# Kernel optimization log

Hardware: AMD Instinct MI355X
Metric: run time of the kernel (lower is better)

## Reference

```python
import jax, jax.numpy as jnp
import numpy as np

B, T, D, K = 4, 2048, 1024, 64


def _spectral_filters(seq_len, k):
    # Hankel matrix Z_ij = 2 / ((i+j)^3 - (i+j)), top-k eig-pairs scaled by sigma^0.25
    e = np.arange(1, seq_len + 1, dtype=np.float64)
    ipj = e[:, None] + e[None, :]
    Z = 2.0 / (ipj ** 3 - ipj)
    sig, phi = np.linalg.eigh(Z)
    sig_k = np.clip(sig[-k:], 1e-9, None)
    return (phi[:, -k:] * sig_k ** 0.25).astype(np.float32)


def setup_inputs() -> dict:
    key = jax.random.key(0)
    ks = jax.random.split(key, 6)
    filt = jnp.asarray(_spectral_filters(T, K))  # [T, K]
    inp = {
        "x": jax.random.normal(ks[0], (B, T, D), dtype=jnp.float32),
        "W_pre": jax.random.normal(ks[1], (D, T), dtype=jnp.float32) / np.sqrt(D),
        "b_pre": jnp.zeros((T,), dtype=jnp.float32),
        "Q_filt": filt,
        "K_filt": jnp.array(filt),
        "W_v": jax.random.normal(ks[2], (D, K), dtype=jnp.float32) / np.sqrt(D),
        "b_v": jnp.zeros((K,), dtype=jnp.float32),
        "W_o": jax.random.normal(ks[3], (K, D), dtype=jnp.float32) / np.sqrt(K),
        "b_o": jnp.zeros((D,), dtype=jnp.float32),
        "decay": jnp.ones((T,), dtype=jnp.float32),
    }
    return inp


def reference(x, W_pre, b_pre, Q_filt, K_filt, W_v, b_v, W_o, b_o, decay):
    # pre-projection d_model -> seq_len (since d_model != seq_len)
    x_proj = x @ W_pre + b_pre                      # [B, T, T]
    Q = jnp.einsum('bti,ik->btk', x_proj, Q_filt)   # [B, T, K]
    Kf = jnp.einsum('bti,ik->btk', x_proj, K_filt)  # [B, T, K]
    V = x @ W_v + b_v                               # [B, T, K]
    # outer-product state with per-timestep decay, prefix-summed over time
    Z = jnp.einsum('btp,btn->btpn', V, Kf) * decay[None, :, None, None]  # [B,T,K,K]
    H = jnp.cumsum(Z, axis=1)                       # [B, T, K, K]
    Y = jnp.einsum('btk,btkn->btn', Q, H)           # [B, T, K]
    return Y @ W_o + b_o                            # [B, T, D]
```

## Files before the change

kernel.cpp:

```cpp
#include <hip/hip_runtime.h>

#define TS 2048
#define DM 1024
#define KD 64
#define NB 4

#define WTH_OFF 0
#define WTL_OFF 98304
#define BC_OFF  196608
#define QG_OFF  196864
#define P_OFF   1769728
#define PF_OFF  (P_OFF)
#define ST_OFF  (P_OFF)
#define O_OFF   8061184
#define YB_OFF  9109760

typedef __attribute__((ext_vector_type(8))) short bf16x8;
typedef __attribute__((ext_vector_type(4))) float f32x4;

__device__ __forceinline__ ushort f2bf(float f) {
  unsigned u = __float_as_uint(f);
  unsigned r = u + 0x7FFFu + ((u >> 16) & 1u);
  return (ushort)(r >> 16);
}
__device__ __forceinline__ float bf2f(ushort h) {
  return __uint_as_float(((unsigned)h) << 16);
}

__global__ __launch_bounds__(256) void k_prep(
    const float* __restrict__ W_pre, const float* __restrict__ Qf,
    const float* __restrict__ Kf, float* __restrict__ Pf) {
  const int d0 = blockIdx.x * 64;
  const int f = blockIdx.y;
  const int ks = blockIdx.z;
  const float* __restrict__ F = f ? Kf : Qf;
  const int tid = threadIdx.x;
  const int wave = tid >> 6, lane = tid & 63;
  const int quad = lane >> 4, l15 = lane & 15;
  __shared__ ushort As[64 * 72];
  __shared__ ushort Bs[64 * 72];
  f32x4 acc[4];
#pragma unroll
  for (int nt = 0; nt < 4; ++nt) acc[nt] = (f32x4){0.f, 0.f, 0.f, 0.f};

  const int ra = tid >> 3;
  const int c4 = (tid & 7) * 4;
  float4 aw[2];
  float bw[8];
  int t0 = ks * 128;
#pragma unroll
  for (int i = 0; i < 2; ++i)
    aw[i] = *(const float4*)&W_pre[(size_t)(d0 + i * 32 + ra) * TS + t0 + c4];
#pragma unroll
  for (int h = 0; h < 2; ++h)
#pragma unroll
    for (int u = 0; u < 4; ++u)
      bw[h * 4 + u] = F[(size_t)(t0 + (wave + 4 * h) * 4 + u) * KD + lane];

  for (int step = 0; step < 4; ++step) {
    __syncthreads();
#pragma unroll
    for (int i = 0; i < 2; ++i) {
      const int r = i * 32 + ra;
      const float4 v = aw[i];
      const ushort h0 = f2bf(v.x), h1 = f2bf(v.y), h2 = f2bf(v.z), h3 = f2bf(v.w);
      *(ushort4*)&As[r * 72 + c4] = make_ushort4(h0, h1, h2, h3);
      *(ushort4*)&As[r * 72 + 32 + c4] = make_ushort4(
          f2bf(v.x - bf2f(h0)), f2bf(v.y - bf2f(h1)),
          f2bf(v.z - bf2f(h2)), f2bf(v.w - bf2f(h3)));
    }
#pragma unroll
    for (int h = 0; h < 2; ++h) {
      const int gg = wave + 4 * h;
      ushort hh[4], ll[4];
#pragma unroll
      for (int u = 0; u < 4; ++u) {
        hh[u] = f2bf(bw[h * 4 + u]);
        ll[u] = f2bf(bw[h * 4 + u] - bf2f(hh[u]));
      }
      *(ushort4*)&Bs[lane * 72 + gg * 4] = make_ushort4(hh[0], hh[1], hh[2], hh[3]);
      *(ushort4*)&Bs[lane * 72 + 32 + gg * 4] = make_ushort4(ll[0], ll[1], ll[2], ll[3]);
    }
    __syncthreads();
    if (step < 3) {
      const int t1 = t0 + 32;
#pragma unroll
      for (int i = 0; i < 2; ++i)
        aw[i] = *(const float4*)&W_pre[(size_t)(d0 + i * 32 + ra) * TS + t1 + c4];
#pragma unroll
      for (int h = 0; h < 2; ++h)
#pragma unroll
        for (int u = 0; u < 4; ++u)
          bw[h * 4 + u] = F[(size_t)(t1 + (wave + 4 * h) * 4 + u) * KD + lane];
    }
    const ushort* ap = &As[(wave * 16 + l15) * 72 + quad * 8];
    const bf16x8 a_h = *(const bf16x8*)ap;
    const bf16x8 a_l = *(const bf16x8*)(ap + 32);
#pragma unroll
    for (int nt = 0; nt < 4; ++nt) {
      const ushort* bp = &Bs[(nt * 16 + l15) * 72 + quad * 8];
      const bf16x8 b_h = *(const bf16x8*)bp;
      const bf16x8 b_l = *(const bf16x8*)(bp + 32);
      acc[nt] = __builtin_amdgcn_mfma_f32_16x16x32_bf16(a_h, b_h, acc[nt], 0, 0, 0);
      acc[nt] = __builtin_amdgcn_mfma_f32_16x16x32_bf16(a_h, b_l, acc[nt], 0, 0, 0);
      acc[nt] = __builtin_amdgcn_mfma_f32_16x16x32_bf16(a_l, b_h, acc[nt], 0, 0, 0);
    }
    t0 += 32;
  }
#pragma unroll
  for (int nt = 0; nt < 4; ++nt) {
    const int n = f * 64 + nt * 16 + l15;
#pragma unroll
    for (int r = 0; r < 4; ++r) {
      const int d = d0 + wave * 16 + quad * 4 + r;
      Pf[((size_t)ks * 128 + n) * DM + d] = acc[nt][r];
    }
  }
}

__global__ __launch_bounds__(256) void k_fred(
    const float* __restrict__ Pf, const float* __restrict__ Wv,
    const float* __restrict__ b_pre, const float* __restrict__ Qf,
    const float* __restrict__ Kf, const float* __restrict__ bv,
    ushort* __restrict__ WT_hi, ushort* __restrict__ WT_lo,
    float* __restrict__ bcomb) {
  const int bx = blockIdx.x;
  const int tid = threadIdx.x;
  if (bx < 32) {
    const int n0 = bx * 4;
    const int d4 = tid * 4;
#pragma unroll
    for (int j = 0; j < 4; ++j) {
      const int n = n0 + j;
      float4 s = {0.f, 0.f, 0.f, 0.f};
#pragma unroll
      for (int ks = 0; ks < 16; ++ks) {
        const float4 v = *(const float4*)&Pf[((size_t)ks * 128 + n) * DM + d4];
        s.x += v.x; s.y += v.y; s.z += v.z; s.w += v.w;
      }
      const ushort h0 = f2bf(s.x), h1 = f2bf(s.y), h2 = f2bf(s.z), h3 = f2bf(s.w);
      *(ushort4*)&WT_hi[(size_t)n * DM + d4] = make_ushort4(h0, h1, h2, h3);
      *(ushort4*)&WT_lo[(size_t)n * DM + d4] = make_ushort4(
          f2bf(s.x - bf2f(h0)), f2bf(s.y - bf2f(h1)),
          f2bf(s.z - bf2f(h2)), f2bf(s.w - bf2f(h3)));
    }
    const float* __restrict__ F = (n0 < 64) ? Qf : Kf;
    const int c0 = n0 & 63;
    __shared__ float bred[4][256];
    float p[4] = {0.f, 0.f, 0.f, 0.f};
#pragma unroll
    for (int u = 0; u < 8; ++u) {
      const int t = tid * 8 + u;
      const float bp = b_pre[t];
#pragma unroll
      for (int j = 0; j < 4; ++j) p[j] += bp * F[(size_t)t * KD + c0 + j];
    }
#pragma unroll
    for (int j = 0; j < 4; ++j) bred[j][tid] = p[j];
    __syncthreads();
    for (int s = 128; s > 0; s >>= 1) {
      if (tid < s) {
#pragma unroll
        for (int j = 0; j < 4; ++j) bred[j][tid] += bred[j][tid + s];
      }
      __syncthreads();
    }
    if (tid < 4) bcomb[n0 + tid] = bred[tid][0];
  } else {
    const int n0 = 128 + (bx - 32) * 4;
    const int d4 = tid * 4;
#pragma unroll
    for (int j = 0; j < 4; ++j) {
      const int c = n0 - 128 + j;
      float v[4];
#pragma unroll
      for (int i = 0; i < 4; ++i) v[i] = Wv[(size_t)(d4 + i) * KD + c];
      const ushort h0 = f2bf(v[0]), h1 = f2bf(v[1]), h2 = f2bf(v[2]), h3 = f2bf(v[3]);
      *(ushort4*)&WT_hi[(size_t)(n0 + j) * DM + d4] = make_ushort4(h0, h1, h2, h3);
      *(ushort4*)&WT_lo[(size_t)(n0 + j) * DM + d4] = make_ushort4(
          f2bf(v[0] - bf2f(h0)), f2bf(v[1] - bf2f(h1)),
          f2bf(v[2] - bf2f(h2)), f2bf(v[3] - bf2f(h3)));
    }
    if (tid < 4) bcomb[n0 + tid] = bv[n0 - 128 + tid];
  }
}

__global__ __launch_bounds__(256) void k_qkv(
    const float* __restrict__ x, const ushort* __restrict__ WT_hi,
    const ushort* __restrict__ WT_lo, float* __restrict__ P) {
  const int row0 = blockIdx.x * 64;
  const int ks = blockIdx.y;
  const int tid = threadIdx.x;
  const int wave = tid >> 6, lane = tid & 63;
  const int quad = lane >> 4, l15 = lane & 15;
  const int n0 = wave * 48;
  __shared__ ushort As[64 * 72];
  __shared__ ushort Bs[192 * 72];
  f32x4 acc[4][3];
#pragma unroll
  for (int mt = 0; mt < 4; ++mt)
#pragma unroll
    for (int nt = 0; nt < 3; ++nt) acc[mt][nt] = (f32x4){0.f, 0.f, 0.f, 0.f};

  for (int step = 0; step < 8; ++step) {
    const int kk = ks * 256 + step * 32;
    __syncthreads();
#pragma unroll
    for (int i = 0; i < 2; ++i) {
      const int idx = i * 256 + tid;
      const int r = idx >> 3, c4 = (idx & 7) * 4;
      const float4 v = *(const float4*)&x[(size_t)(row0 + r) * DM + kk + c4];
      const ushort h0 = f2bf(v.x), h1 = f2bf(v.y), h2 = f2bf(v.z), h3 = f2bf(v.w);
      *(ushort4*)&As[r * 72 + c4] = make_ushort4(h0, h1, h2, h3);
      *(ushort4*)&As[r * 72 + 32 + c4] = make_ushort4(
          f2bf(v.x - bf2f(h0)), f2bf(v.y - bf2f(h1)),
          f2bf(v.z - bf2f(h2)), f2bf(v.w - bf2f(h3)));
    }
#pragma unroll
    for (int i = 0; i < 6; ++i) {
      const int idx = i * 256 + tid;
      const int half = idx >= 768;
      const int j = half ? idx - 768 : idx;
      const int n = j >> 2, ch = j & 3;
      const ushort* src = (half ? WT_lo : WT_hi) + (size_t)n * DM + kk + ch * 8;
      *(float4*)&Bs[n * 72 + half * 32 + ch * 8] = *(const float4*)src;
    }
    __syncthreads();
    bf16x8 a_h[4], a_l[4], b_h[3], b_l[3];
#pragma unroll
    for (int mt = 0; mt < 4; ++mt) {
      const ushort* p = &As[(mt * 16 + l15) * 72 + quad * 8];
      a_h[mt] = *(const bf16x8*)p;
      a_l[mt] = *(const bf16x8*)(p + 32);
    }
#pragma unroll
    for (int nt = 0; nt < 3; ++nt) {
      const ushort* p = &Bs[(n0 + nt * 16 + l15) * 72 + quad * 8];
      b_h[nt] = *(const bf16x8*)p;
      b_l[nt] = *(const bf16x8*)(p + 32);
    }
#pragma unroll
    for (int mt = 0; mt < 4; ++mt)
#pragma unroll
      for (int nt = 0; nt < 3; ++nt) {
        acc[mt][nt] = __builtin_amdgcn_mfma_f32_16x16x32_bf16(a_h[mt], b_h[nt], acc[mt][nt], 0, 0, 0);
        acc[mt][nt] = __builtin_amdgcn_mfma_f32_16x16x32_bf16(a_h[mt], b_l[nt], acc[mt][nt], 0, 0, 0);
        acc[mt][nt] = __builtin_amdgcn_mfma_f32_16x16x32_bf16(a_l[mt], b_h[nt], acc[mt][nt], 0, 0, 0);
      }
  }
  float* Pp = P + (size_t)ks * TS * NB * 192;
#pragma unroll
  for (int mt = 0; mt < 4; ++mt) {
    const int rbase = row0 + mt * 16 + quad * 4;
#pragma unroll
    for (int nt = 0; nt < 3; ++nt) {
      const int col = n0 + nt * 16 + l15;
#pragma unroll
      for (int r = 0; r < 4; ++r)
        Pp[(size_t)(rbase + r) * 192 + col] = acc[mt][nt][r];
    }
  }
}

__global__ __launch_bounds__(256) void k_chunkred(
    const float* __restrict__ P, const float* __restrict__ bcomb,
    const float* __restrict__ decay, float* __restrict__ Qg,
    float* __restrict__ Yb, float* __restrict__ O) {
  const int c = blockIdx.x;
  const int b = blockIdx.y;
  const int s0 = c * 32;
  const int tid = threadIdx.x;
  __shared__ float Qs[32][68], Ks[32][68], Vs[32][68];
  __shared__ float Ss[32][36];
  __shared__ float dec[32];
  const size_t NTOT = (size_t)TS * NB * 192;

  for (int idx = tid; idx < 32 * 48; idx += 256) {
    const int r = idx / 48, cq = (idx % 48) * 4;
    const size_t g = (size_t)(b * TS + s0 + r) * 192 + cq;
    float4 a = *(const float4*)&P[g];
    const float4 b2 = *(const float4*)&P[NTOT + g];
    const float4 c2 = *(const float4*)&P[2 * NTOT + g];
    const float4 d2 = *(const float4*)&P[3 * NTOT + g];
    const float4 bi = *(const float4*)&bcomb[cq];
    a.x += b2.x + c2.x + d2.x + bi.x;
    a.y += b2.y + c2.y + d2.y + bi.y;
    a.z += b2.z + c2.z + d2.z + bi.z;
    a.w += b2.w + c2.w + d2.w + bi.w;
    if (cq < 64) {
      *(float4*)&Qs[r][cq] = a;
      *(float4*)&Qg[(size_t)(b * TS + s0 + r) * KD + cq] = a;
    } else if (cq < 128) {
      *(float4*)&Ks[r][cq - 64] = a;
    } else {
      *(float4*)&Vs[r][cq - 128] = a;
    }
  }
  if (tid < 32) dec[tid] = decay[s0 + tid];
  __syncthreads();

  {
    const int sc = (tid & 15) * 2;
    const int tr = (tid >> 4) * 2;
    float a00 = 0.f, a01 = 0.f, a10 = 0.f, a11 = 0.f;
#pragma unroll
    for (int k = 0; k < 64; k += 4) {
      const float4 q0 = *(const float4*)&Qs[tr][k];
      const float4 q1 = *(const float4*)&Qs[tr + 1][k];
      const float4 v0 = *(const float4*)&Vs[sc][k];
      const float4 v1 = *(const float4*)&Vs[sc + 1][k];
      a00 += q0.x * v0.x + q0.y * v0.y + q0.z * v0.z + q0.w * v0.w;
      a01 += q0.x * v1.x + q0.y * v1.y + q0.z * v1.z + q0.w * v1.w;
      a10 += q1.x * v0.x + q1.y * v0.y + q1.z * v0.z + q1.w * v0.w;
      a11 += q1.x * v1.x + q1.y * v1.y + q1.z * v1.z + q1.w * v1.w;
    }
    const float d0 = dec[sc], d1 = dec[sc + 1];
    Ss[tr][sc]         = (sc     <= tr)     ? a00 * d0 : 0.f;
    Ss[tr][sc + 1]     = (sc + 1 <= tr)     ? a01 * d1 : 0.f;
    Ss[tr + 1][sc]     = (sc     <= tr + 1) ? a10 * d0 : 0.f;
    Ss[tr + 1][sc + 1] = (sc + 1 <= tr + 1) ? a11 * d1 : 0.f;
  }

  float o[4][4];
#pragma unroll
  for (int i = 0; i < 4; ++i)
#pragma unroll
    for (int j = 0; j < 4; ++j) o[i][j] = 0.f;
  {
    const int kx = (tid & 15) * 4;
    const int nx = (tid >> 4) * 4;
#pragma unroll
    for (int s = 0; s < 32; ++s) {
      const float ds = dec[s];
      float4 v4 = *(const float4*)&Vs[s][kx];
      const float4 k4 = *(const float4*)&Ks[s][nx];
      v4.x *= ds; v4.y *= ds; v4.z *= ds; v4.w *= ds;
      o[0][0] += v4.x * k4.x; o[0][1] += v4.x * k4.y; o[0][2] += v4.x * k4.z; o[0][3] += v4.x * k4.w;
      o[1][0] += v4.y * k4.x; o[1][1] += v4.y * k4.y; o[1][2] += v4.y * k4.z; o[1][3] += v4.y * k4.w;
      o[2][0] += v4.z * k4.x; o[2][1] += v4.z * k4.y; o[2][2] += v4.z * k4.z; o[2][3] += v4.z * k4.w;
      o[3][0] += v4.w * k4.x; o[3][1] += v4.w * k4.y; o[3][2] += v4.w * k4.z; o[3][3] += v4.w * k4.w;
    }
  }
  __syncthreads();

  {
    const int nx = (tid & 15) * 4;
    const int tr = (tid >> 4) * 2;
    float y0[4] = {0.f, 0.f, 0.f, 0.f};
    float y1[4] = {0.f, 0.f, 0.f, 0.f};
#pragma unroll
    for (int s = 0; s < 32; s += 4) {
      const float4 sa = *(const float4*)&Ss[tr][s];
      const float4 sb = *(const float4*)&Ss[tr + 1][s];
#pragma unroll
      for (int u = 0; u < 4; ++u) {
        const float4 k4 = *(const float4*)&Ks[s + u][nx];
        const float su0 = (u == 0) ? sa.x : (u == 1) ? sa.y : (u == 2) ? sa.z : sa.w;
        const float su1 = (u == 0) ? sb.x : (u == 1) ? sb.y : (u == 2) ? sb.z : sb.w;
        y0[0] += su0 * k4.x; y0[1] += su0 * k4.y; y0[2] += su0 * k4.z; y0[3] += su0 * k4.w;
        y1[0] += su1 * k4.x; y1[1] += su1 * k4.y; y1[2] += su1 * k4.z; y1[3] += su1 * k4.w;
      }
    }
    float4 w0, w1;
    w0.x = y0[0]; w0.y = y0[1]; w0.z = y0[2]; w0.w = y0[3];
    w1.x = y1[0]; w1.y = y1[1]; w1.z = y1[2]; w1.w = y1[3];
    *(float4*)&Yb[(size_t)(b * TS + s0 + tr) * KD + nx] = w0;
    *(float4*)&Yb[(size_t)(b * TS + s0 + tr + 1) * KD + nx] = w1;
  }

  {
    const int kx = (tid & 15) * 4;
    const int nx = (tid >> 4) * 4;
    const size_t base = ((size_t)(b * 64 + c) * 64) * 64;
#pragma unroll
    for (int i = 0; i < 4; ++i) {
      float4 w;
      w.x = o[i][0]; w.y = o[i][1]; w.z = o[i][2]; w.w = o[i][3];
      *(float4*)&O[base + (size_t)(kx + i) * 64 + nx] = w;
    }
  }
}

__global__ __launch_bounds__(256) void k_scan(const float* __restrict__ O,
                                              float* __restrict__ St) {
  const int e = blockIdx.x * 256 + threadIdx.x;
  const int b = blockIdx.y;
  const float* op = O + (size_t)b * 64 * 4096 + e;
  float* sp = St + (size_t)b * 64 * 4096 + e;
  float run = 0.f;
  for (int c = 0; c < 64; ++c) {
    sp[(size_t)c * 4096] = run;
    run += op[(size_t)c * 4096];
  }
}

__global__ __launch_bounds__(512) void k_interout(
    const float* __restrict__ St, const float* __restrict__ Qg,
    const float* __restrict__ Yb, const float* __restrict__ Wo,
    const float* __restrict__ bo, float* __restrict__ out) {
  const int c = blockIdx.x;
  const int b = blockIdx.y;
  const int z = blockIdx.z;
  const int t0 = c * 32;
  const int tid = threadIdx.x;
  __shared__ float Sts[64][68];
  __shared__ float Qs[32][68];
  __shared__ float Yrow[32][68];

  {
    const size_t sb = ((size_t)b * 64 + c) * 4096;
#pragma unroll
    for (int g = 0; g < 2; ++g) {
      const int idx = g * 512 + tid;
      const int k = idx >> 4, n = (idx & 15) * 4;
      *(float4*)&Sts[k][n] = *(const float4*)&St[sb + (size_t)k * 64 + n];
    }
  }
  {
    const int r = tid >> 4, q = (tid & 15) * 4;
    *(float4*)&Qs[r][q] = *(const float4*)&Qg[(size_t)(b * TS + t0 + r) * KD + q];
    *(float4*)&Yrow[r][q] = *(const float4*)&Yb[(size_t)(b * TS + t0 + r) * KD + q];
  }
  __syncthreads();

  {
    const int nx = (tid & 15) * 4;
    const int tr = tid >> 4;
    float y0[4] = {0.f, 0.f, 0.f, 0.f};
#pragma unroll
    for (int k = 0; k < 64; k += 4) {
      const float4 q0 = *(const float4*)&Qs[tr][k];
#pragma unroll
      for (int u = 0; u < 4; ++u) {
        const float4 s4 = *(const float4*)&Sts[k + u][nx];
        const float a0 = (u == 0) ? q0.x : (u == 1) ? q0.y : (u == 2) ? q0.z : q0.w;
        y0[0] += a0 * s4.x; y0[1] += a0 * s4.y; y0[2] += a0 * s4.z; y0[3] += a0 * s4.w;
      }
    }
    float4 p0 = *(const float4*)&Yrow[tr][nx];
    p0.x += y0[0]; p0.y += y0[1]; p0.z += y0[2]; p0.w += y0[3];
    *(float4*)&Yrow[tr][nx] = p0;
  }
  __syncthreads();

  const int rg = (tid >> 6) * 4;
  const int dcol = z * 256 + (tid & 63) * 4;
  const float4 b4 = *(const float4*)&bo[dcol];
  float acc[4][4];
#pragma unroll
  for (int r = 0; r < 4; ++r)
#pragma unroll
    for (int j = 0; j < 4; ++j) acc[r][j] = 0.f;
#pragma unroll 8
  for (int k = 0; k < 64; ++k) {
    const float4 w4 = *(const float4*)&Wo[(size_t)k * DM + dcol];
    const float y0 = Yrow[rg + 0][k];
    const float y1 = Yrow[rg + 1][k];
    const float y2 = Yrow[rg + 2][k];
    const float y3 = Yrow[rg + 3][k];
    acc[0][0] += y0 * w4.x; acc[0][1] += y0 * w4.y; acc[0][2] += y0 * w4.z; acc[0][3] += y0 * w4.w;
    acc[1][0] += y1 * w4.x; acc[1][1] += y1 * w4.y; acc[1][2] += y1 * w4.z; acc[1][3] += y1 * w4.w;
    acc[2][0] += y2 * w4.x; acc[2][1] += y2 * w4.y; acc[2][2] += y2 * w4.z; acc[2][3] += y2 * w4.w;
    acc[3][0] += y3 * w4.x; acc[3][1] += y3 * w4.y; acc[3][2] += y3 * w4.z; acc[3][3] += y3 * w4.w;
  }
#pragma unroll
  for (int r = 0; r < 4; ++r) {
    float4 w;
    w.x = acc[r][0] + b4.x;
    w.y = acc[r][1] + b4.y;
    w.z = acc[r][2] + b4.z;
    w.w = acc[r][3] + b4.w;
    *(float4*)&out[(size_t)(b * TS + t0 + rg + r) * DM + dcol] = w;
  }
}

extern "C" void kernel_launch(void* const* d_in, const int* in_sizes, int n_in,
                              void* d_out, int out_size, void* d_ws, size_t ws_size,
                              hipStream_t stream) {
  const float* x     = (const float*)d_in[0];
  const float* W_pre = (const float*)d_in[1];
  const float* b_pre = (const float*)d_in[2];
  const float* Qf    = (const float*)d_in[3];
  const float* Kf    = (const float*)d_in[4];
  const float* W_v   = (const float*)d_in[5];
  const float* b_v   = (const float*)d_in[6];
  const float* W_o   = (const float*)d_in[7];
  const float* b_o   = (const float*)d_in[8];
  const float* decay = (const float*)d_in[9];
  float* out = (float*)d_out;
  float* ws = (float*)d_ws;

  ushort* WT_hi = (ushort*)(ws + WTH_OFF);
  ushort* WT_lo = (ushort*)(ws + WTL_OFF);
  float* bcomb = ws + BC_OFF;
  float* Qg    = ws + QG_OFF;
  float* P     = ws + P_OFF;
  float* Pf    = ws + PF_OFF;
  float* St    = ws + ST_OFF;
  float* O     = ws + O_OFF;
  float* Yb    = ws + YB_OFF;

  k_prep<<<dim3(16, 2, 16), 256, 0, stream>>>(W_pre, Qf, Kf, Pf);
  k_fred<<<dim3(48), 256, 0, stream>>>(Pf, W_v, b_pre, Qf, Kf, b_v,
                                       WT_hi, WT_lo, bcomb);
  k_qkv<<<dim3(NB * TS / 64, 4), 256, 0, stream>>>(x, WT_hi, WT_lo, P);
  k_chunkred<<<dim3(TS / 32, NB), 256, 0, stream>>>(P, bcomb, decay, Qg, Yb, O);
  k_scan<<<dim3(16, NB), 256, 0, stream>>>(O, St);
  k_interout<<<dim3(TS / 32, NB, 4), 512, 0, stream>>>(St, Qg, Yb, W_o, b_o, out);
}
```

Baseline: 179.0 us.

## Split inter-chunk and output projection, run output GEMM on bf16x3 MFMA

Splits the fused inter-chunk/output kernel in two. The new inter-chunk kernel computes Y once per chunk instead of once per output column slice, and stores it as hi/lo bf16 pairs. A new output kernel does Y @ W_o with split-bf16 MFMA, using a transposed hi/lo copy of W_o built in the prep kernel. This removes the redundant Y recomputation across the four z slices and the scalar FP32 FMA work. It adds one extra launch and a round trip of Y through global memory, and the output stores go out as scattered scalar writes.

```diff
diff --git a/kernel.cpp b/kernel.cpp
--- a/kernel.cpp
+++ b/kernel.cpp
@@ -14,6 +14,10 @@
 #define ST_OFF  (P_OFF)
 #define O_OFF   8061184
 #define YB_OFF  9109760
+#define WOTH_OFF 9634048
+#define WOTL_OFF 9666816
+#define YFH_OFF  9699584
+#define YFL_OFF  9961728
 
 typedef __attribute__((ext_vector_type(8))) short bf16x8;
 typedef __attribute__((ext_vector_type(4))) float f32x4;
@@ -122,8 +126,10 @@
     const float* __restrict__ Pf, const float* __restrict__ Wv,
     const float* __restrict__ b_pre, const float* __restrict__ Qf,
     const float* __restrict__ Kf, const float* __restrict__ bv,
+    const float* __restrict__ Wo,
     ushort* __restrict__ WT_hi, ushort* __restrict__ WT_lo,
-    float* __restrict__ bcomb) {
+    float* __restrict__ bcomb,
+    ushort* __restrict__ WoT_hi, ushort* __restrict__ WoT_lo) {
   const int bx = blockIdx.x;
   const int tid = threadIdx.x;
   if (bx < 32) {
@@ -166,7 +172,7 @@
       __syncthreads();
     }
     if (tid < 4) bcomb[n0 + tid] = bred[tid][0];
-  } else {
+  } else if (bx < 48) {
     const int n0 = 128 + (bx - 32) * 4;
     const int d4 = tid * 4;
 #pragma unroll
@@ -182,6 +188,18 @@
           f2bf(v[2] - bf2f(h2)), f2bf(v[3] - bf2f(h3)));
     }
     if (tid < 4) bcomb[n0 + tid] = bv[n0 - 128 + tid];
+  } else {
+    const int d0 = (bx - 48) * 64;
+    const int d = d0 + (tid >> 2);
+    const int k0 = (tid & 3) * 16;
+#pragma unroll
+    for (int u = 0; u < 16; ++u) {
+      const int k = k0 + u;
+      const float v = Wo[(size_t)k * DM + d];
+      const ushort h = f2bf(v);
+      WoT_hi[(size_t)d * KD + k] = h;
+      WoT_lo[(size_t)d * KD + k] = f2bf(v - bf2f(h));
+    }
   }
 }
 
@@ -394,83 +412,122 @@
   }
 }
 
-__global__ __launch_bounds__(512) void k_interout(
+__global__ __launch_bounds__(256) void k_inter(
     const float* __restrict__ St, const float* __restrict__ Qg,
-    const float* __restrict__ Yb, const float* __restrict__ Wo,
-    const float* __restrict__ bo, float* __restrict__ out) {
+    const float* __restrict__ Yb, ushort* __restrict__ Yh,
+    ushort* __restrict__ Yl) {
   const int c = blockIdx.x;
   const int b = blockIdx.y;
-  const int z = blockIdx.z;
   const int t0 = c * 32;
   const int tid = threadIdx.x;
   __shared__ float Sts[64][68];
   __shared__ float Qs[32][68];
-  __shared__ float Yrow[32][68];
-
   {
     const size_t sb = ((size_t)b * 64 + c) * 4096;
 #pragma unroll
-    for (int g = 0; g < 2; ++g) {
-      const int idx = g * 512 + tid;
+    for (int g = 0; g < 4; ++g) {
+      const int idx = g * 256 + tid;
       const int k = idx >> 4, n = (idx & 15) * 4;
       *(float4*)&Sts[k][n] = *(const float4*)&St[sb + (size_t)k * 64 + n];
     }
-  }
-  {
-    const int r = tid >> 4, q = (tid & 15) * 4;
-    *(float4*)&Qs[r][q] = *(const float4*)&Qg[(size_t)(b * TS + t0 + r) * KD + q];
-    *(float4*)&Yrow[r][q] = *(const float4*)&Yb[(size_t)(b * TS + t0 + r) * KD + q];
+#pragma unroll
+    for (int g = 0; g < 2; ++g) {
+      const int idx = g * 256 + tid;
+      const int r = idx >> 4, q = (idx & 15) * 4;
+      *(float4*)&Qs[r][q] = *(const float4*)&Qg[(size_t)(b * TS + t0 + r) * KD + q];
+    }
   }
   __syncthreads();
 
-  {
-    const int nx = (tid & 15) * 4;
-    const int tr = tid >> 4;
-    float y0[4] = {0.f, 0.f, 0.f, 0.f};
-#pragma unroll
-    for (int k = 0; k < 64; k += 4) {
-      const float4 q0 = *(const float4*)&Qs[tr][k];
-#pragma unroll
-      for (int u = 0; u < 4; ++u) {
-        const float4 s4 = *(const float4*)&Sts[k + u][nx];
-        const float a0 = (u == 0) ? q0.x : (u == 1) ? q0.y : (u == 2) ? q0.z : q0.w;
-        y0[0] += a0 * s4.x; y0[1] += a0 * s4.y; y0[2] += a0 * s4.z; y0[3] += a0 * s4.w;
+  const int nx = (tid & 15) * 4;
+  const int tr = tid >> 4;
+  float y0[4] = {0.f, 0.f, 0.f, 0.f};
+  float y1[4] = {0.f, 0.f, 0.f, 0.f};
+#pragma unroll
+  for (int k = 0; k < 64; k += 4) {
+    const float4 q0 = *(const float4*)&Qs[tr][k];
+    const float4 q1 = *(const float4*)&Qs[tr + 16][k];
+#pragma unroll
+    for (int u = 0; u < 4; ++u) {
+      const float4 s4 = *(const float4*)&Sts[k + u][nx];
+      const float a0 = (u == 0) ? q0.x : (u == 1) ? q0.y : (u == 2) ? q0.z : q0.w;
+      const float a1 = (u == 0) ? q1.x : (u == 1) ? q1.y : (u == 2) ? q1.z : q1.w;
+      y0[0] += a0 * s4.x; y0[1] += a0 * s4.y; y0[2] += a0 * s4.z; y0[3] += a0 * s4.w;
+      y1[0] += a1 * s4.x; y1[1] += a1 * s4.y; y1[2] += a1 * s4.z; y1[3] += a1 * s4.w;
+    }
+  }
+
+  const size_t r0 = (size_t)(b * TS + t0 + tr) * KD + nx;
+  const size_t r1 = (size_t)(b * TS + t0 + tr + 16) * KD + nx;
+  float4 p0 = *(const float4*)&Yb[r0];
+  float4 p1 = *(const float4*)&Yb[r1];
+  p0.x += y0[0]; p0.y += y0[1]; p0.z += y0[2]; p0.w += y0[3];
+  p1.x += y1[0]; p1.y += y1[1]; p1.z += y1[2]; p1.w += y1[3];
+  const ushort h00 = f2bf(p0.x), h01 = f2bf(p0.y), h02 = f2bf(p0.z), h03 = f2bf(p0.w);
+  const ushort h10 = f2bf(p1.x), h11 = f2bf(p1.y), h12 = f2bf(p1.z), h13 = f2bf(p1.w);
+  *(ushort4*)&Yh[r0] = make_ushort4(h00, h01, h02, h03);
+  *(ushort4*)&Yl[r0] = make_ushort4(
+      f2bf(p0.x - bf2f(h00)), f2bf(p0.y - bf2f(h01)),
+      f2bf(p0.z - bf2f(h02)), f2bf(p0.w - bf2f(h03)));
+  *(ushort4*)&Yh[r1] = make_ushort4(h10, h11, h12, h13);
+  *(ushort4*)&Yl[r1] = make_ushort4(
+      f2bf(p1.x - bf2f(h10)), f2bf(p1.y - bf2f(h11)),
+      f2bf(p1.z - bf2f(h12)), f2bf(p1.w - bf2f(h13)));
+}
+
+__global__ __launch_bounds__(256) void k_out(
+    const ushort* __restrict__ Yh, const ushort* __restrict__ Yl,
+    const ushort* __restrict__ Wh, const ushort* __restrict__ Wl,
+    const float* __restrict__ bo, float* __restrict__ out) {
+  const int m0 = blockIdx.x * 64;
+  const int tid = threadIdx.x;
+  const int wave = tid >> 6, lane = tid & 63;
+  const int quad = lane >> 4, l15 = lane & 15;
+  const int n0 = blockIdx.y * 256 + wave * 64;
+
+  bf16x8 a_h[4][2], a_l[4][2];
+#pragma unroll
+  for (int mt = 0; mt < 4; ++mt)
+#pragma unroll
+    for (int kk = 0; kk < 2; ++kk) {
+      const size_t off = (size_t)(m0 + mt * 16 + l15) * KD + kk * 32 + quad * 8;
+      a_h[mt][kk] = *(const bf16x8*)&Yh[off];
+      a_l[mt][kk] = *(const bf16x8*)&Yl[off];
+    }
+
+  f32x4 acc[4][4];
+#pragma unroll
+  for (int mt = 0; mt < 4; ++mt)
+#pragma unroll
+    for (int nt = 0; nt < 4; ++nt) acc[mt][nt] = (f32x4){0.f, 0.f, 0.f, 0.f};
+
+#pragma unroll
+  for (int nt = 0; nt < 4; ++nt) {
+#pragma unroll
+    for (int kk = 0; kk < 2; ++kk) {
+      const size_t off = (size_t)(n0 + nt * 16 + l15) * KD + kk * 32 + quad * 8;
+      const bf16x8 b_h = *(const bf16x8*)&Wh[off];
+      const bf16x8 b_l = *(const bf16x8*)&Wl[off];
+#pragma unroll
+      for (int mt = 0; mt < 4; ++mt) {
+        acc[mt][nt] = __builtin_amdgcn_mfma_f32_16x16x32_bf16(a_h[mt][kk], b_h, acc[mt][nt], 0, 0, 0);
+        acc[mt][nt] = __builtin_amdgcn_mfma_f32_16x16x32_bf16(a_h[mt][kk], b_l, acc[mt][nt], 0, 0, 0);
+        acc[mt][nt] = __builtin_amdgcn_mfma_f32_16x16x32_bf16(a_l[mt][kk], b_h, acc[mt][nt], 0, 0, 0);
       }
     }
-    float4 p0 = *(const float4*)&Yrow[tr][nx];
-    p0.x += y0[0]; p0.y += y0[1]; p0.z += y0[2]; p0.w += y0[3];
-    *(float4*)&Yrow[tr][nx] = p0;
-  }
-  __syncthreads();
-
-  const int rg = (tid >> 6) * 4;
-  const int dcol = z * 256 + (tid & 63) * 4;
-  const float4 b4 = *(const float4*)&bo[dcol];
-  float acc[4][4];
-#pragma unroll
-  for (int r = 0; r < 4; ++r)
-#pragma unroll
-    for (int j = 0; j < 4; ++j) acc[r][j] = 0.f;
-#pragma unroll 8
-  for (int k = 0; k < 64; ++k) {
-    const float4 w4 = *(const float4*)&Wo[(size_t)k * DM + dcol];
-    const float y0 = Yrow[rg + 0][k];
-    const float y1 = Yrow[rg + 1][k];
-    const float y2 = Yrow[rg + 2][k];
-    const float y3 = Yrow[rg + 3][k];
-    acc[0][0] += y0 * w4.x; acc[0][1] += y0 * w4.y; acc[0][2] += y0 * w4.z; acc[0][3] += y0 * w4.w;
-    acc[1][0] += y1 * w4.x; acc[1][1] += y1 * w4.y; acc[1][2] += y1 * w4.z; acc[1][3] += y1 * w4.w;
-    acc[2][0] += y2 * w4.x; acc[2][1] += y2 * w4.y; acc[2][2] += y2 * w4.z; acc[2][3] += y2 * w4.w;
-    acc[3][0] += y3 * w4.x; acc[3][1] += y3 * w4.y; acc[3][2] += y3 * w4.z; acc[3][3] += y3 * w4.w;
-  }
-#pragma unroll
-  for (int r = 0; r < 4; ++r) {
-    float4 w;
-    w.x = acc[r][0] + b4.x;
-    w.y = acc[r][1] + b4.y;
-    w.z = acc[r][2] + b4.z;
-    w.w = acc[r][3] + b4.w;
-    *(float4*)&out[(size_t)(b * TS + t0 + rg + r) * DM + dcol] = w;
+  }
+
+#pragma unroll
+  for (int nt = 0; nt < 4; ++nt) {
+    const int col = n0 + nt * 16 + l15;
+    const float bb = bo[col];
+#pragma unroll
+    for (int mt = 0; mt < 4; ++mt) {
+      const int rbase = m0 + mt * 16 + quad * 4;
+#pragma unroll
+      for (int r = 0; r < 4; ++r)
+        out[(size_t)(rbase + r) * DM + col] = acc[mt][nt][r] + bb;
+    }
   }
 }
 
@@ -499,12 +556,18 @@
   float* St    = ws + ST_OFF;
   float* O     = ws + O_OFF;
   float* Yb    = ws + YB_OFF;
+  ushort* WoT_hi = (ushort*)(ws + WOTH_OFF);
+  ushort* WoT_lo = (ushort*)(ws + WOTL_OFF);
+  ushort* Yf_hi  = (ushort*)(ws + YFH_OFF);
+  ushort* Yf_lo  = (ushort*)(ws + YFL_OFF);
 
   k_prep<<<dim3(16, 2, 16), 256, 0, stream>>>(W_pre, Qf, Kf, Pf);
-  k_fred<<<dim3(48), 256, 0, stream>>>(Pf, W_v, b_pre, Qf, Kf, b_v,
-                                       WT_hi, WT_lo, bcomb);
+  k_fred<<<dim3(64), 256, 0, stream>>>(Pf, W_v, b_pre, Qf, Kf, b_v, W_o,
+                                       WT_hi, WT_lo, bcomb, WoT_hi, WoT_lo);
   k_qkv<<<dim3(NB * TS / 64, 4), 256, 0, stream>>>(x, WT_hi, WT_lo, P);
   k_chunkred<<<dim3(TS / 32, NB), 256, 0, stream>>>(P, bcomb, decay, Qg, Yb, O);
   k_scan<<<dim3(16, NB), 256, 0, stream>>>(O, St);
-  k_interout<<<dim3(TS / 32, NB, 4), 512, 0, stream>>>(St, Qg, Yb, W_o, b_o, out);
-}
+  k_inter<<<dim3(TS / 32, NB), 256, 0, stream>>>(St, Qg, Yb, Yf_hi, Yf_lo);
+  k_out<<<dim3(NB * TS / 64, 4), 256, 0, stream>>>(Yf_hi, Yf_lo, WoT_hi, WoT_lo,
+                                                   b_o, out);
+}
```

Result: faster. 170.7 us (-4.6%).
